# Kernel optimization log

Hardware: AMD Instinct MI355X
Metric: run time of the kernel (lower is better)

Reference implementation:

```python
import jax, jax.numpy as jnp
import numpy as np

N = 8192
IN_F = 256
OUT_F = 128


def setup_inputs() -> dict:
    key = jax.random.key(0)
    k1, k2, k3, k4, k5, k6 = jax.random.split(key, 6)
    input = jax.random.normal(k1, (N, IN_F), dtype=jnp.float32)
    adj = jax.random.randint(k2, (N, N), 0, 2, dtype=jnp.int32)
    # xavier-uniform-like init scaled by gain=0.5
    def xavier(k, shape, gain=0.5):
        fan_in, fan_out = shape[0], shape[1]
        lim = gain * np.sqrt(6.0 / (fan_in + fan_out))
        return jax.random.uniform(k, shape, dtype=jnp.float32, minval=-lim, maxval=lim)
    W_s = xavier(k3, (IN_F, OUT_F))
    a_s = xavier(k4, (OUT_F, 1))
    W_n = xavier(k5, (IN_F, OUT_F))
    a_n = xavier(k6, (OUT_F, 1))
    return {"input": input, "adj": adj, "W_s": W_s, "a_s": a_s, "W_n": W_n, "a_n": a_n}


def reference(input, adj, W_s, a_s, W_n, a_n):
    # Projections: [N, out_features]
    h_s = input @ W_s
    h_n = input @ W_n
    # Additive attention logits: e[i, j] = relu((h_s @ a_s)[i] + (h_n @ a_n)[j])
    e = jax.nn.relu((h_s @ a_s) + (h_n @ a_n).T)  # [N, N]
    # Masked softmax over neighbors (dim=1)
    attention = jnp.where(adj > 0, e, jnp.float32(-9e15))
    attention = jax.nn.softmax(attention, axis=1)
    # Self-scaling term (sum of softmax rows, kept for faithfulness)
    attention_sum = jnp.sum(attention, axis=-1, keepdims=True)
    attention_s = 1.0 / (1.0 + attention_sum)
    # Dropout is identity in eval mode (p=0 / training=False)
    h_prime = attention_s * h_s + attention @ h_n
    # concat=True -> elu activation
    return jax.nn.elu(h_prime)
```

## Files before the change

kernel.cpp:

```cpp
#include <hip/hip_runtime.h>
#include <math.h>

#define NN 8192

typedef short short8 __attribute__((ext_vector_type(8)));
typedef float f32x4 __attribute__((ext_vector_type(4)));

__device__ __forceinline__ float eluf(float x) {
  return x > 0.f ? x : (__expf(x) - 1.f);
}
__device__ __forceinline__ unsigned short f2bf(float f) {
  union { float f; unsigned u; } v; v.f = f;
  unsigned r = v.u + 0x7fffu + ((v.u >> 16) & 1u);
  return (unsigned short)(r >> 16);
}

__global__ __launch_bounds__(256) void k_proj(const float* __restrict__ X,
                                              const float* __restrict__ Ws,
                                              const float* __restrict__ Wn,
                                              const float* __restrict__ as_,
                                              const float* __restrict__ an_,
                                              float* __restrict__ Hs,
                                              unsigned short* __restrict__ HnT,
                                              float* __restrict__ s_out,
                                              float* __restrict__ n_out) {
  __shared__ float4 lin4[8 * 64];
  const int t = threadIdx.x;
  const int i0 = blockIdx.x * 8;
  const float4* Xg = (const float4*)X + (size_t)i0 * 64;
  lin4[t] = Xg[t];
  if (t < 256) lin4[t + 256] = Xg[t + 256];
  __syncthreads();
  const int c = t & 127;
  const int rh = t >> 7;
  float accs[4], accn[4];
#pragma unroll
  for (int r = 0; r < 4; ++r) { accs[r] = 0.f; accn[r] = 0.f; }
  for (int k = 0; k < 256; k += 4) {
    float ws0 = Ws[(k + 0) * 128 + c], ws1 = Ws[(k + 1) * 128 + c];
    float ws2 = Ws[(k + 2) * 128 + c], ws3 = Ws[(k + 3) * 128 + c];
    float wn0 = Wn[(k + 0) * 128 + c], wn1 = Wn[(k + 1) * 128 + c];
    float wn2 = Wn[(k + 2) * 128 + c], wn3 = Wn[(k + 3) * 128 + c];
#pragma unroll
    for (int r = 0; r < 4; ++r) {
      float4 iv = lin4[(rh * 4 + r) * 64 + (k >> 2)];
      accs[r] = fmaf(iv.x, ws0, accs[r]); accs[r] = fmaf(iv.y, ws1, accs[r]);
      accs[r] = fmaf(iv.z, ws2, accs[r]); accs[r] = fmaf(iv.w, ws3, accs[r]);
      accn[r] = fmaf(iv.x, wn0, accn[r]); accn[r] = fmaf(iv.y, wn1, accn[r]);
      accn[r] = fmaf(iv.z, wn2, accn[r]); accn[r] = fmaf(iv.w, wn3, accn[r]);
    }
  }
#pragma unroll
  for (int r = 0; r < 4; ++r)
    Hs[(size_t)(i0 + rh * 4 + r) * 128 + c] = accs[r];
  {
    union { unsigned short us[4]; ushort4 u4; } pk;
#pragma unroll
    for (int r = 0; r < 4; ++r) pk.us[r] = f2bf(accn[r]);
    *(ushort4*)(HnT + (size_t)c * NN + i0 + rh * 4) = pk.u4;
  }
  float* red = (float*)lin4;
  const int wv = t >> 6, ln = t & 63;
  __syncthreads();
  {
    float av = as_[c];
#pragma unroll
    for (int r = 0; r < 4; ++r) red[(rh * 4 + r) * 128 + c] = accs[r] * av;
  }
  __syncthreads();
#pragma unroll
  for (int h = 0; h < 2; ++h) {
    int row = wv * 2 + h;
    float p = red[row * 128 + ln] + red[row * 128 + 64 + ln];
#pragma unroll
    for (int off = 32; off >= 1; off >>= 1) p += __shfl_down(p, off);
    if (ln == 0) s_out[i0 + row] = p;
  }
  __syncthreads();
  {
    float av = an_[c];
#pragma unroll
    for (int r = 0; r < 4; ++r) red[(rh * 4 + r) * 128 + c] = accn[r] * av;
  }
  __syncthreads();
#pragma unroll
  for (int h = 0; h < 2; ++h) {
    int row = wv * 2 + h;
    float p = red[row * 128 + ln] + red[row * 128 + 64 + ln];
#pragma unroll
    for (int off = 32; off >= 1; off >>= 1) p += __shfl_down(p, off);
    if (ln == 0) n_out[i0 + row] = p;
  }
}

__global__ __launch_bounds__(256) void k_main(const int* __restrict__ A,
                                              const unsigned short* __restrict__ HnT,
                                              const float* __restrict__ sv_g,
                                              const float* __restrict__ nv_g,
                                              float* __restrict__ HsOut) {
  __shared__ short8 fragbuf[2][4][64];
  __shared__ float zsh[64];
  __shared__ float zf[16];

  const int t = threadIdx.x;
  const int wv = t >> 6;
  const int ln = t & 63;
  const int q = ln >> 4;
  const int m = ln & 15;
  const int row0 = blockIdx.x * 16;

  const float sm = sv_g[row0 + m];
  const int jlane = wv * 32 + q * 8;
  const int* aptr = A + (size_t)(row0 + m) * NN + jlane;
  const float* nptr = nv_g + jlane;

  const int f0 = wv * 32 + m;
  const unsigned short* bb0 = HnT + (size_t)f0 * NN + q * 8;
  const unsigned short* bb1 = HnT + (size_t)(f0 + 16) * NN + q * 8;

  f32x4 acc0 = {0.f, 0.f, 0.f, 0.f}, acc1 = {0.f, 0.f, 0.f, 0.f};
  float zp = 0.f;

  int4 adjv[2][2];
  float4 nvv[2][2];
  union { uint4 u; short8 s; } breg[8];
  adjv[0][0] = *(const int4*)(aptr);       adjv[0][1] = *(const int4*)(aptr + 4);
  adjv[1][0] = *(const int4*)(aptr + 128); adjv[1][1] = *(const int4*)(aptr + 132);
  nvv[0][0] = *(const float4*)(nptr);      nvv[0][1] = *(const float4*)(nptr + 4);
  breg[0].u = *(const uint4*)(bb0);        breg[1].u = *(const uint4*)(bb0 + 32);
  breg[2].u = *(const uint4*)(bb0 + 64);   breg[3].u = *(const uint4*)(bb0 + 96);
  breg[4].u = *(const uint4*)(bb1);        breg[5].u = *(const uint4*)(bb1 + 32);
  breg[6].u = *(const uint4*)(bb1 + 64);   breg[7].u = *(const uint4*)(bb1 + 96);

#pragma unroll 2
  for (int tt = 0; tt < 64; ++tt) {
    const int cur = tt & 1;
    {
      float nvl[8] = {nvv[cur][0].x, nvv[cur][0].y, nvv[cur][0].z, nvv[cur][0].w,
                      nvv[cur][1].x, nvv[cur][1].y, nvv[cur][1].z, nvv[cur][1].w};
      int av[8] = {adjv[cur][0].x, adjv[cur][0].y, adjv[cur][0].z, adjv[cur][0].w,
                   adjv[cur][1].x, adjv[cur][1].y, adjv[cur][1].z, adjv[cur][1].w};
      short8 fr;
#pragma unroll
      for (int k = 0; k < 8; ++k) {
        float w = av[k] > 0 ? __expf(fmaxf(sm + nvl[k], 0.f)) : 0.f;
        zp += w;
        fr[k] = (short)f2bf(w);
      }
      fragbuf[cur][wv][ln] = fr;
    }
    if (tt < 62) {
      const int* p = aptr + (tt + 2) * 128;
      adjv[cur][0] = *(const int4*)p;
      adjv[cur][1] = *(const int4*)(p + 4);
    }
    if (tt < 63) {
      const float* p = nptr + (tt + 1) * 128;
      nvv[cur ^ 1][0] = *(const float4*)p;
      nvv[cur ^ 1][1] = *(const float4*)(p + 4);
    }
    __syncthreads();
    short8 a0 = fragbuf[cur][0][ln];
    short8 a1 = fragbuf[cur][1][ln];
    short8 a2 = fragbuf[cur][2][ln];
    short8 a3 = fragbuf[cur][3][ln];
    acc0 = __builtin_amdgcn_mfma_f32_16x16x32_bf16(a0, breg[0].s, acc0, 0, 0, 0);
    acc1 = __builtin_amdgcn_mfma_f32_16x16x32_bf16(a0, breg[4].s, acc1, 0, 0, 0);
    acc0 = __builtin_amdgcn_mfma_f32_16x16x32_bf16(a1, breg[1].s, acc0, 0, 0, 0);
    acc1 = __builtin_amdgcn_mfma_f32_16x16x32_bf16(a1, breg[5].s, acc1, 0, 0, 0);
    acc0 = __builtin_amdgcn_mfma_f32_16x16x32_bf16(a2, breg[2].s, acc0, 0, 0, 0);
    acc1 = __builtin_amdgcn_mfma_f32_16x16x32_bf16(a2, breg[6].s, acc1, 0, 0, 0);
    acc0 = __builtin_amdgcn_mfma_f32_16x16x32_bf16(a3, breg[3].s, acc0, 0, 0, 0);
    acc1 = __builtin_amdgcn_mfma_f32_16x16x32_bf16(a3, breg[7].s, acc1, 0, 0, 0);
    if (tt < 63) {
      const size_t jt = (size_t)(tt + 1) * 128;
      breg[0].u = *(const uint4*)(bb0 + jt);      breg[1].u = *(const uint4*)(bb0 + jt + 32);
      breg[2].u = *(const uint4*)(bb0 + jt + 64); breg[3].u = *(const uint4*)(bb0 + jt + 96);
      breg[4].u = *(const uint4*)(bb1 + jt);      breg[5].u = *(const uint4*)(bb1 + jt + 32);
      breg[6].u = *(const uint4*)(bb1 + jt + 64); breg[7].u = *(const uint4*)(bb1 + jt + 96);
    }
  }

  {
    float zz = zp;
    zz += __shfl_down(zz, 32);
    zz += __shfl_down(zz, 16);
    if (ln < 16) zsh[wv * 16 + ln] = zz;
  }
  __syncthreads();
  if (t < 16) zf[t] = 1.f / (zsh[t] + zsh[16 + t] + zsh[32 + t] + zsh[48 + t]);
  __syncthreads();

#pragma unroll
  for (int reg = 0; reg < 4; ++reg) {
    const int row = q * 4 + reg;
    const float invz = zf[row];
    const size_t off = (size_t)(row0 + row) * 128 + f0;
    float h0 = HsOut[off], h1 = HsOut[off + 16];
    HsOut[off]      = eluf(fmaf(acc0[reg], invz, 0.5f * h0));
    HsOut[off + 16] = eluf(fmaf(acc1[reg], invz, 0.5f * h1));
  }
}

extern "C" void kernel_launch(void* const* d_in, const int* in_sizes, int n_in,
                              void* d_out, int out_size, void* d_ws, size_t ws_size,
                              hipStream_t stream) {
  const float* X   = (const float*)d_in[0];
  const int*   A   = (const int*)d_in[1];
  const float* Ws  = (const float*)d_in[2];
  const float* as_ = (const float*)d_in[3];
  const float* Wn  = (const float*)d_in[4];
  const float* an_ = (const float*)d_in[5];
  float* out = (float*)d_out;

  unsigned short* HnT = (unsigned short*)d_ws;
  float* s = (float*)(HnT + (size_t)128 * NN);
  float* n = s + NN;

  k_proj<<<1024, 256, 0, stream>>>(X, Ws, Wn, as_, an_, out, HnT, s, n);
  k_main<<<512, 256, 0, stream>>>(A, HnT, s, n, out);
}
```

Before: 466.0 us.

## Factor exp of relu into per-node exponentials and drop LDS exchange

```diff
diff --git a/kernel.cpp b/kernel.cpp
--- a/kernel.cpp
+++ b/kernel.cpp
@@ -1,4 +1,5 @@
 #include <hip/hip_runtime.h>
+#include <hip/hip_bf16.h>
 #include <math.h>
 
 #define NN 8192
@@ -22,8 +23,8 @@
                                               const float* __restrict__ an_,
                                               float* __restrict__ Hs,
                                               unsigned short* __restrict__ HnT,
-                                              float* __restrict__ s_out,
-                                              float* __restrict__ n_out) {
+                                              float* __restrict__ es_out,
+                                              float* __restrict__ en_out) {
   __shared__ float4 lin4[8 * 64];
   const int t = threadIdx.x;
   const int i0 = blockIdx.x * 8;
@@ -74,7 +75,7 @@
     float p = red[row * 128 + ln] + red[row * 128 + 64 + ln];
 #pragma unroll
     for (int off = 32; off >= 1; off >>= 1) p += __shfl_down(p, off);
-    if (ln == 0) s_out[i0 + row] = p;
+    if (ln == 0) es_out[i0 + row] = __expf(p);
   }
   __syncthreads();
   {
@@ -89,19 +90,15 @@
     float p = red[row * 128 + ln] + red[row * 128 + 64 + ln];
 #pragma unroll
     for (int off = 32; off >= 1; off >>= 1) p += __shfl_down(p, off);
-    if (ln == 0) n_out[i0 + row] = p;
-  }
-}
-
-__global__ __launch_bounds__(256) void k_main(const int* __restrict__ A,
-                                              const unsigned short* __restrict__ HnT,
-                                              const float* __restrict__ sv_g,
-                                              const float* __restrict__ nv_g,
-                                              float* __restrict__ HsOut) {
-  __shared__ short8 fragbuf[2][4][64];
-  __shared__ float zsh[64];
-  __shared__ float zf[16];
-
+    if (ln == 0) en_out[i0 + row] = __expf(p);
+  }
+}
+
+__global__ __launch_bounds__(256, 2) void k_main(const int* __restrict__ A,
+                                                 const unsigned short* __restrict__ HnT,
+                                                 const float* __restrict__ es_g,
+                                                 const float* __restrict__ en_g,
+                                                 float* __restrict__ HsOut) {
   const int t = threadIdx.x;
   const int wv = t >> 6;
   const int ln = t & 63;
@@ -109,11 +106,9 @@
   const int m = ln & 15;
   const int row0 = blockIdx.x * 16;
 
-  const float sm = sv_g[row0 + m];
-  const int jlane = wv * 32 + q * 8;
-  const int* aptr = A + (size_t)(row0 + m) * NN + jlane;
-  const float* nptr = nv_g + jlane;
-
+  const float es = es_g[row0 + m];
+  const int* aptr = A + (size_t)(row0 + m) * NN + q * 8;
+  const float* nptr = en_g + q * 8;
   const int f0 = wv * 32 + m;
   const unsigned short* bb0 = HnT + (size_t)f0 * NN + q * 8;
   const unsigned short* bb1 = HnT + (size_t)(f0 + 16) * NN + q * 8;
@@ -121,84 +116,107 @@
   f32x4 acc0 = {0.f, 0.f, 0.f, 0.f}, acc1 = {0.f, 0.f, 0.f, 0.f};
   float zp = 0.f;
 
-  int4 adjv[2][2];
-  float4 nvv[2][2];
-  union { uint4 u; short8 s; } breg[8];
-  adjv[0][0] = *(const int4*)(aptr);       adjv[0][1] = *(const int4*)(aptr + 4);
-  adjv[1][0] = *(const int4*)(aptr + 128); adjv[1][1] = *(const int4*)(aptr + 132);
-  nvv[0][0] = *(const float4*)(nptr);      nvv[0][1] = *(const float4*)(nptr + 4);
-  breg[0].u = *(const uint4*)(bb0);        breg[1].u = *(const uint4*)(bb0 + 32);
-  breg[2].u = *(const uint4*)(bb0 + 64);   breg[3].u = *(const uint4*)(bb0 + 96);
-  breg[4].u = *(const uint4*)(bb1);        breg[5].u = *(const uint4*)(bb1 + 32);
-  breg[6].u = *(const uint4*)(bb1 + 64);   breg[7].u = *(const uint4*)(bb1 + 96);
+  int4 adjv[2][4][2];
+  float4 env[2][4][2];
+  union BU { uint4 u; short8 s; } breg[8];
+
+#pragma unroll
+  for (int ks = 0; ks < 4; ++ks) {
+    adjv[0][ks][0] = *(const int4*)(aptr + ks * 32);
+    adjv[0][ks][1] = *(const int4*)(aptr + ks * 32 + 4);
+  }
+#pragma unroll
+  for (int ks = 0; ks < 4; ++ks) {
+    env[0][ks][0] = *(const float4*)(nptr + ks * 32);
+    env[0][ks][1] = *(const float4*)(nptr + ks * 32 + 4);
+  }
+#pragma unroll
+  for (int ks = 0; ks < 4; ++ks) {
+    adjv[1][ks][0] = *(const int4*)(aptr + 128 + ks * 32);
+    adjv[1][ks][1] = *(const int4*)(aptr + 128 + ks * 32 + 4);
+  }
+#pragma unroll
+  for (int ks = 0; ks < 4; ++ks) {
+    env[1][ks][0] = *(const float4*)(nptr + 128 + ks * 32);
+    env[1][ks][1] = *(const float4*)(nptr + 128 + ks * 32 + 4);
+  }
+#pragma unroll
+  for (int ks = 0; ks < 4; ++ks) {
+    breg[ks].u     = *(const uint4*)(bb0 + ks * 32);
+    breg[4 + ks].u = *(const uint4*)(bb1 + ks * 32);
+  }
 
 #pragma unroll 2
   for (int tt = 0; tt < 64; ++tt) {
     const int cur = tt & 1;
-    {
-      float nvl[8] = {nvv[cur][0].x, nvv[cur][0].y, nvv[cur][0].z, nvv[cur][0].w,
-                      nvv[cur][1].x, nvv[cur][1].y, nvv[cur][1].z, nvv[cur][1].w};
-      int av[8] = {adjv[cur][0].x, adjv[cur][0].y, adjv[cur][0].z, adjv[cur][0].w,
-                   adjv[cur][1].x, adjv[cur][1].y, adjv[cur][1].z, adjv[cur][1].w};
-      short8 fr;
-#pragma unroll
-      for (int k = 0; k < 8; ++k) {
-        float w = av[k] > 0 ? __expf(fmaxf(sm + nvl[k], 0.f)) : 0.f;
-        zp += w;
-        fr[k] = (short)f2bf(w);
+    short8 afr[4];
+#pragma unroll
+    for (int ks = 0; ks < 4; ++ks) {
+      const int4 a0 = adjv[cur][ks][0], a1 = adjv[cur][ks][1];
+      const float4 e0 = env[cur][ks][0], e1 = env[cur][ks][1];
+      float w0 = a0.x > 0 ? fmaxf(es * e0.x, 1.f) : 0.f;
+      float w1 = a0.y > 0 ? fmaxf(es * e0.y, 1.f) : 0.f;
+      float w2 = a0.z > 0 ? fmaxf(es * e0.z, 1.f) : 0.f;
+      float w3 = a0.w > 0 ? fmaxf(es * e0.w, 1.f) : 0.f;
+      float w4 = a1.x > 0 ? fmaxf(es * e1.x, 1.f) : 0.f;
+      float w5 = a1.y > 0 ? fmaxf(es * e1.y, 1.f) : 0.f;
+      float w6 = a1.z > 0 ? fmaxf(es * e1.z, 1.f) : 0.f;
+      float w7 = a1.w > 0 ? fmaxf(es * e1.w, 1.f) : 0.f;
+      zp += ((w0 + w1) + (w2 + w3)) + ((w4 + w5) + (w6 + w7));
+      __hip_bfloat162 p01 = __float22bfloat162_rn(float2{w0, w1});
+      __hip_bfloat162 p23 = __float22bfloat162_rn(float2{w2, w3});
+      __hip_bfloat162 p45 = __float22bfloat162_rn(float2{w4, w5});
+      __hip_bfloat162 p67 = __float22bfloat162_rn(float2{w6, w7});
+      union { unsigned u[4]; short8 s; } fr;
+      fr.u[0] = *(unsigned*)&p01; fr.u[1] = *(unsigned*)&p23;
+      fr.u[2] = *(unsigned*)&p45; fr.u[3] = *(unsigned*)&p67;
+      afr[ks] = fr.s;
+    }
+    if (tt < 62) {
+      const int* ap = aptr + (size_t)(tt + 2) * 128;
+      const float* np = nptr + (size_t)(tt + 2) * 128;
+#pragma unroll
+      for (int ks = 0; ks < 4; ++ks) {
+        adjv[cur][ks][0] = *(const int4*)(ap + ks * 32);
+        adjv[cur][ks][1] = *(const int4*)(ap + ks * 32 + 4);
       }
-      fragbuf[cur][wv][ln] = fr;
-    }
-    if (tt < 62) {
-      const int* p = aptr + (tt + 2) * 128;
-      adjv[cur][0] = *(const int4*)p;
-      adjv[cur][1] = *(const int4*)(p + 4);
-    }
-    if (tt < 63) {
-      const float* p = nptr + (tt + 1) * 128;
-      nvv[cur ^ 1][0] = *(const float4*)p;
-      nvv[cur ^ 1][1] = *(const float4*)(p + 4);
-    }
-    __syncthreads();
-    short8 a0 = fragbuf[cur][0][ln];
-    short8 a1 = fragbuf[cur][1][ln];
-    short8 a2 = fragbuf[cur][2][ln];
-    short8 a3 = fragbuf[cur][3][ln];
-    acc0 = __builtin_amdgcn_mfma_f32_16x16x32_bf16(a0, breg[0].s, acc0, 0, 0, 0);
-    acc1 = __builtin_amdgcn_mfma_f32_16x16x32_bf16(a0, breg[4].s, acc1, 0, 0, 0);
-    acc0 = __builtin_amdgcn_mfma_f32_16x16x32_bf16(a1, breg[1].s, acc0, 0, 0, 0);
-    acc1 = __builtin_amdgcn_mfma_f32_16x16x32_bf16(a1, breg[5].s, acc1, 0, 0, 0);
-    acc0 = __builtin_amdgcn_mfma_f32_16x16x32_bf16(a2, breg[2].s, acc0, 0, 0, 0);
-    acc1 = __builtin_amdgcn_mfma_f32_16x16x32_bf16(a2, breg[6].s, acc1, 0, 0, 0);
-    acc0 = __builtin_amdgcn_mfma_f32_16x16x32_bf16(a3, breg[3].s, acc0, 0, 0, 0);
-    acc1 = __builtin_amdgcn_mfma_f32_16x16x32_bf16(a3, breg[7].s, acc1, 0, 0, 0);
+#pragma unroll
+      for (int ks = 0; ks < 4; ++ks) {
+        env[cur][ks][0] = *(const float4*)(np + ks * 32);
+        env[cur][ks][1] = *(const float4*)(np + ks * 32 + 4);
+      }
+    }
+    acc0 = __builtin_amdgcn_mfma_f32_16x16x32_bf16(afr[0], breg[0].s, acc0, 0, 0, 0);
+    acc1 = __builtin_amdgcn_mfma_f32_16x16x32_bf16(afr[0], breg[4].s, acc1, 0, 0, 0);
+    acc0 = __builtin_amdgcn_mfma_f32_16x16x32_bf16(afr[1], breg[1].s, acc0, 0, 0, 0);
+    acc1 = __builtin_amdgcn_mfma_f32_16x16x32_bf16(afr[1], breg[5].s, acc1, 0, 0, 0);
+    acc0 = __builtin_amdgcn_mfma_f32_16x16x32_bf16(afr[2], breg[2].s, acc0, 0, 0, 0);
+    acc1 = __builtin_amdgcn_mfma_f32_16x16x32_bf16(afr[2], breg[6].s, acc1, 0, 0, 0);
+    acc0 = __builtin_amdgcn_mfma_f32_16x16x32_bf16(afr[3], breg[3].s, acc0, 0, 0, 0);
+    acc1 = __builtin_amdgcn_mfma_f32_16x16x32_bf16(afr[3], breg[7].s, acc1, 0, 0, 0);
     if (tt < 63) {
       const size_t jt = (size_t)(tt + 1) * 128;
-      breg[0].u = *(const uint4*)(bb0 + jt);      breg[1].u = *(const uint4*)(bb0 + jt + 32);
-      breg[2].u = *(const uint4*)(bb0 + jt + 64); breg[3].u = *(const uint4*)(bb0 + jt + 96);
-      breg[4].u = *(const uint4*)(bb1 + jt);      breg[5].u = *(const uint4*)(bb1 + jt + 32);
-      breg[6].u = *(const uint4*)(bb1 + jt + 64); breg[7].u = *(const uint4*)(bb1 + jt + 96);
-    }
-  }
-
-  {
-    float zz = zp;
-    zz += __shfl_down(zz, 32);
-    zz += __shfl_down(zz, 16);
-    if (ln < 16) zsh[wv * 16 + ln] = zz;
-  }
-  __syncthreads();
-  if (t < 16) zf[t] = 1.f / (zsh[t] + zsh[16 + t] + zsh[32 + t] + zsh[48 + t]);
-  __syncthreads();
+#pragma unroll
+      for (int ks = 0; ks < 4; ++ks) {
+        breg[ks].u     = *(const uint4*)(bb0 + jt + ks * 32);
+        breg[4 + ks].u = *(const uint4*)(bb1 + jt + ks * 32);
+      }
+    }
+  }
+
+  float zz = zp;
+  zz += __shfl_xor(zz, 16);
+  zz += __shfl_xor(zz, 32);
+  const float invz = 1.f / zz;
 
 #pragma unroll
   for (int reg = 0; reg < 4; ++reg) {
     const int row = q * 4 + reg;
-    const float invz = zf[row];
+    const float iz = __shfl(invz, row);
     const size_t off = (size_t)(row0 + row) * 128 + f0;
     float h0 = HsOut[off], h1 = HsOut[off + 16];
-    HsOut[off]      = eluf(fmaf(acc0[reg], invz, 0.5f * h0));
-    HsOut[off + 16] = eluf(fmaf(acc1[reg], invz, 0.5f * h1));
+    HsOut[off]      = eluf(fmaf(acc0[reg], iz, 0.5f * h0));
+    HsOut[off + 16] = eluf(fmaf(acc1[reg], iz, 0.5f * h1));
   }
 }
 
@@ -214,9 +232,9 @@
   float* out = (float*)d_out;
 
   unsigned short* HnT = (unsigned short*)d_ws;
-  float* s = (float*)(HnT + (size_t)128 * NN);
-  float* n = s + NN;
-
-  k_proj<<<1024, 256, 0, stream>>>(X, Ws, Wn, as_, an_, out, HnT, s, n);
-  k_main<<<512, 256, 0, stream>>>(A, HnT, s, n, out);
-}
+  float* es = (float*)(HnT + (size_t)128 * NN);
+  float* en = es + NN;
+
+  k_proj<<<1024, 256, 0, stream>>>(X, Ws, Wn, as_, an_, out, HnT, es, en);
+  k_main<<<512, 256, 0, stream>>>(A, HnT, es, en, out);
+}
```

Result: slower. 785.0 us (+68.5%).
